# Kernel tuning notes

Measured on AMD Instinct MI355X. Metric: run time of the kernel, lower is better.

## Reference

```python
import jax, jax.numpy as jnp
import numpy as np

# dims
B, S, D, H, F = 4, 1024, 1024, 16, 4096
DH = D // H
THETA0 = 1.0   # base firing threshold of AdaptiveLIFNeuron
RHO = 0.9      # adaptation decay
EPS = 1e-5


def layer_norm(x, g, b):
    mu = jnp.mean(x, axis=-1, keepdims=True)
    var = jnp.mean((x - mu) ** 2, axis=-1, keepdims=True)
    return (x - mu) * jax.lax.rsqrt(var + EPS) * g + b


def spike(u):
    # Heaviside forward, sigmoid surrogate gradient (straight-through)
    sg = jax.nn.sigmoid(4.0 * u)
    hard = (u > 0).astype(u.dtype)
    return sg + jax.lax.stop_gradient(hard - sg)


def setup_inputs() -> dict:
    key = jax.random.key(0)
    ks = jax.random.split(key, 8)
    std = 0.02
    w = lambda k, shape: jax.random.normal(k, shape, jnp.float32) * std
    return {
        "x": jax.random.normal(ks[0], (B, S, D), jnp.float32),
        "Wq": w(ks[1], (D, D)), "bq": jnp.zeros((D,), jnp.float32),
        "Wk": w(ks[2], (D, D)), "bk": jnp.zeros((D,), jnp.float32),
        "Wv": w(ks[3], (D, D)), "bv": jnp.zeros((D,), jnp.float32),
        "Wo": w(ks[4], (D, D)), "bo": jnp.zeros((D,), jnp.float32),
        "g1": jnp.ones((D,), jnp.float32), "b1": jnp.zeros((D,), jnp.float32),
        "W1": w(ks[5], (D, F)), "bf1": jnp.zeros((F,), jnp.float32),
        "W2": w(ks[6], (F, D)), "bf2": jnp.zeros((D,), jnp.float32),
        "g2": jnp.ones((D,), jnp.float32), "b2": jnp.zeros((D,), jnp.float32),
        "decay": jnp.full((F,), 0.8, jnp.float32),  # per-feature membrane leak
        "beta": jnp.full((F,), 0.1, jnp.float32),   # per-feature threshold adaptation
    }


def reference(x, Wq, bq, Wk, bk, Wv, bv, Wo, bo, g1, b1, W1, bf1, W2, bf2, g2, b2, decay, beta):
    # --- causal multi-head self-attention (DSALayer) ---
    q = (x @ Wq + bq).reshape(B, S, H, DH)
    k = (x @ Wk + bk).reshape(B, S, H, DH)
    v = (x @ Wv + bv).reshape(B, S, H, DH)
    scores = jnp.einsum("bqhd,bkhd->bhqk", q, k) / np.sqrt(DH).astype(np.float32)
    causal = jnp.tril(jnp.ones((S, S), bool))
    scores = jnp.where(causal, scores, jnp.asarray(-1e9, scores.dtype))
    p = jax.nn.softmax(scores, axis=-1)
    attn = jnp.einsum("bhqk,bkhd->bqhd", p, v).reshape(B, S, D) @ Wo + bo
    h = layer_norm(x + attn, g1, b1)

    # --- feed-forward with per-timestep adaptive LIF recurrence ---
    ff = h @ W1 + bf1                      # [B, S, F]

    def step(carry, xt):
        vm, a = carry                      # membrane potential, adaptation
        vm = decay * vm + xt
        u = vm - (THETA0 + a)
        s = spike(u)
        vm = vm * (1.0 - s)                # hard reset on spike
        a = RHO * a + beta * s
        return (vm, a), s

    init = (jnp.zeros((B, F), x.dtype), jnp.zeros((B, F), x.dtype))
    _, spikes = jax.lax.scan(step, init, jnp.swapaxes(ff, 0, 1))  # scan over time
    spikes = jnp.swapaxes(spikes, 0, 1)    # [B, S, F]

    ff_out = spikes @ W2 + bf2
    return layer_norm(h + ff_out, g2, b2)
```

## Files before the change

### kernel.cpp

```cpp
#include <hip/hip_runtime.h>
#include <hip/hip_bf16.h>
#include <stdint.h>

#define Bsz 4
#define Ssz 1024
#define Dsz 1024
#define Hsz 16
#define Fsz 4096

typedef __hip_bfloat16 bf16;
typedef __attribute__((ext_vector_type(8))) short bf16x8;
typedef __attribute__((ext_vector_type(4))) float f32x4;

typedef __attribute__((address_space(1))) const void gvoid_t;
typedef __attribute__((address_space(3))) void svoid_t;

__device__ __forceinline__ void gload16(const bf16* g, bf16* l) {
    __builtin_amdgcn_global_load_lds((gvoid_t*)g, (svoid_t*)l, 16, 0, 0);
}

__global__ __launch_bounds__(256) void split_k(const float* __restrict__ src,
                                               bf16* __restrict__ hi,
                                               bf16* __restrict__ lo) {
    const int i = (blockIdx.x * 256 + threadIdx.x) * 4;
    const float4 v = *(const float4*)(src + i);
    float vv[4] = {v.x, v.y, v.z, v.w};
    #pragma unroll
    for (int u = 0; u < 4; ++u) {
        const bf16 h = __float2bfloat16(vv[u]);
        hi[i + u] = h;
        lo[i + u] = __float2bfloat16(vv[u] - __bfloat162float(h));
    }
}

__global__ __launch_bounds__(256) void transpose_split4_k(const float* __restrict__ Wq,
                                                          const float* __restrict__ Wk,
                                                          const float* __restrict__ Wv,
                                                          const float* __restrict__ Wo,
                                                          bf16* __restrict__ qkv_hi,
                                                          bf16* __restrict__ qkv_lo,
                                                          bf16* __restrict__ wo_hi,
                                                          bf16* __restrict__ wo_lo) {
    __shared__ float tile[32][33];
    const int z = blockIdx.z;
    const float* in = (z == 0) ? Wq : (z == 1) ? Wk : (z == 2) ? Wv : Wo;
    const size_t WP = (size_t)Dsz * Dsz;
    bf16* hiT = (z < 3) ? qkv_hi + (size_t)z * WP : wo_hi;
    bf16* loT = (z < 3) ? qkv_lo + (size_t)z * WP : wo_lo;
    const int bx = blockIdx.x * 32, by = blockIdx.y * 32;
    const int tx = threadIdx.x, ty = threadIdx.y;
    #pragma unroll
    for (int i = 0; i < 32; i += 8)
        tile[ty + i][tx] = in[(size_t)(by + ty + i) * Dsz + bx + tx];
    __syncthreads();
    #pragma unroll
    for (int i = 0; i < 32; i += 8) {
        const float v = tile[tx][ty + i];
        const bf16 h = __float2bfloat16(v);
        const size_t o = (size_t)(bx + ty + i) * Dsz + by + tx;
        hiT[o] = h;
        loT[o] = __float2bfloat16(v - __bfloat162float(h));
    }
}

__global__ __launch_bounds__(256) void transpose_split_k(const float* __restrict__ in,
                                                         bf16* __restrict__ hiT,
                                                         bf16* __restrict__ loT,
                                                         int R, int C) {
    __shared__ float tile[32][33];
    const int bx = blockIdx.x * 32, by = blockIdx.y * 32;
    const int tx = threadIdx.x, ty = threadIdx.y;
    #pragma unroll
    for (int i = 0; i < 32; i += 8)
        tile[ty + i][tx] = in[(size_t)(by + ty + i) * C + bx + tx];
    __syncthreads();
    #pragma unroll
    for (int i = 0; i < 32; i += 8) {
        const float v = tile[tx][ty + i];
        const bf16 h = __float2bfloat16(v);
        const size_t o = (size_t)(bx + ty + i) * R + by + tx;
        hiT[o] = h;
        loT[o] = __float2bfloat16(v - __bfloat162float(h));
    }
}

__global__ __launch_bounds__(256) void transpose_cast_k(const float* __restrict__ in,
                                                        bf16* __restrict__ outT,
                                                        int R, int C) {
    __shared__ float tile[32][33];
    const int bx = blockIdx.x * 32, by = blockIdx.y * 32;
    const int tx = threadIdx.x, ty = threadIdx.y;
    #pragma unroll
    for (int i = 0; i < 32; i += 8)
        tile[ty + i][tx] = in[(size_t)(by + ty + i) * C + bx + tx];
    __syncthreads();
    #pragma unroll
    for (int i = 0; i < 32; i += 8)
        outT[(size_t)(bx + ty + i) * R + by + tx] = __float2bfloat16(tile[tx][ty + i]);
}

__global__ __launch_bounds__(256) void gemm3_bt(const bf16* __restrict__ Ah,
                                                const bf16* __restrict__ Al,
                                                const bf16* __restrict__ Bh,
                                                const bf16* __restrict__ Bl,
                                                const float* __restrict__ bias,
                                                float* __restrict__ Cf,
                                                int M, int N, int K) {
    __shared__ alignas(16) bf16 Ash[128 * 32];
    __shared__ alignas(16) bf16 Asl[128 * 32];
    __shared__ alignas(16) bf16 Bsh[128 * 32];
    __shared__ alignas(16) bf16 Bsl[128 * 32];
    const int t = threadIdx.x;
    const int lane = t & 63, wv = t >> 6;
    const int mw = wv >> 1, nw = wv & 1;
    const int m0 = blockIdx.y * 128, n0 = blockIdx.x * 128;
    const int r16 = lane & 15, q8 = (lane >> 4) * 8;
    const int arow = t >> 2, acol = (t & 3) * 8;

    const bf16* gAh = Ah + (size_t)(m0 + arow) * K + acol;
    const bf16* gAl = Al + (size_t)(m0 + arow) * K + acol;
    const bf16* gBh = Bh + (size_t)(n0 + arow) * K + acol;
    const bf16* gBl = Bl + (size_t)(n0 + arow) * K + acol;
    const size_t rK64 = (size_t)64 * K;
    bf16* lAh = Ash + wv * 512;
    bf16* lAl = Asl + wv * 512;
    bf16* lBh = Bsh + wv * 512;
    bf16* lBl = Bsl + wv * 512;

    f32x4 acc[4][4] = {};

    for (int k0 = 0; k0 < K; k0 += 32) {
        __syncthreads();
        gload16(gAh + k0, lAh);  gload16(gAh + k0 + rK64, lAh + 2048);
        gload16(gAl + k0, lAl);  gload16(gAl + k0 + rK64, lAl + 2048);
        gload16(gBh + k0, lBh);  gload16(gBh + k0 + rK64, lBh + 2048);
        gload16(gBl + k0, lBl);  gload16(gBl + k0 + rK64, lBl + 2048);
        __syncthreads();

        bf16x8 ah[4], al[4], bh[4], bl[4];
        #pragma unroll
        for (int rt = 0; rt < 4; ++rt) {
            const int ro = (64 * mw + 16 * rt + r16) * 32 + q8;
            ah[rt] = *(const bf16x8*)(Ash + ro);
            al[rt] = *(const bf16x8*)(Asl + ro);
        }
        #pragma unroll
        for (int ct = 0; ct < 4; ++ct) {
            const int co = (64 * nw + 16 * ct + r16) * 32 + q8;
            bh[ct] = *(const bf16x8*)(Bsh + co);
            bl[ct] = *(const bf16x8*)(Bsl + co);
        }
        #pragma unroll
        for (int rt = 0; rt < 4; ++rt)
            #pragma unroll
            for (int ct = 0; ct < 4; ++ct) {
                acc[rt][ct] = __builtin_amdgcn_mfma_f32_16x16x32_bf16(ah[rt], bh[ct], acc[rt][ct], 0, 0, 0);
                acc[rt][ct] = __builtin_amdgcn_mfma_f32_16x16x32_bf16(ah[rt], bl[ct], acc[rt][ct], 0, 0, 0);
                acc[rt][ct] = __builtin_amdgcn_mfma_f32_16x16x32_bf16(al[rt], bh[ct], acc[rt][ct], 0, 0, 0);
            }
    }

    const int rowi = (lane >> 4) * 4;
    const int coli = lane & 15;
    #pragma unroll
    for (int ct = 0; ct < 4; ++ct) {
        const int col = n0 + 64 * nw + 16 * ct + coli;
        const float bv = bias[col];
        #pragma unroll
        for (int rt = 0; rt < 4; ++rt) {
            const int rowb = m0 + 64 * mw + 16 * rt + rowi;
            #pragma unroll
            for (int r = 0; r < 4; ++r)
                Cf[(size_t)(rowb + r) * N + col] = acc[rt][ct][r] + bv;
        }
    }
}

__global__ __launch_bounds__(256) void gemm3_qkv(const bf16* __restrict__ Ah,
                                                 const bf16* __restrict__ Al,
                                                 const bf16* __restrict__ Bh,
                                                 const bf16* __restrict__ Bl,
                                                 const float* __restrict__ bias,
                                                 bf16* __restrict__ qhi, bf16* __restrict__ qlo,
                                                 bf16* __restrict__ khi, bf16* __restrict__ klo,
                                                 bf16* __restrict__ vthi, bf16* __restrict__ vtlo) {
    const int K = Dsz;
    __shared__ alignas(16) bf16 Ash[128 * 32];
    __shared__ alignas(16) bf16 Asl[128 * 32];
    __shared__ alignas(16) bf16 Bsh[128 * 32];
    __shared__ alignas(16) bf16 Bsl[128 * 32];
    const int t = threadIdx.x;
    const int lane = t & 63, wv = t >> 6;
    const int mw = wv >> 1, nw = wv & 1;
    const int m0 = blockIdx.y * 128, n0 = blockIdx.x * 128;
    const int r16 = lane & 15, q8 = (lane >> 4) * 8;
    const int arow = t >> 2, acol = (t & 3) * 8;

    const bf16* gAh = Ah + (size_t)(m0 + arow) * K + acol;
    const bf16* gAl = Al + (size_t)(m0 + arow) * K + acol;
    const bf16* gBh = Bh + (size_t)(n0 + arow) * K + acol;
    const bf16* gBl = Bl + (size_t)(n0 + arow) * K + acol;
    const size_t rK64 = (size_t)64 * K;
    bf16* lAh = Ash + wv * 512;
    bf16* lAl = Asl + wv * 512;
    bf16* lBh = Bsh + wv * 512;
    bf16* lBl = Bsl + wv * 512;

    f32x4 acc[4][4] = {};

    for (int k0 = 0; k0 < K; k0 += 32) {
        __syncthreads();
        gload16(gAh + k0, lAh);  gload16(gAh + k0 + rK64, lAh + 2048);
        gload16(gAl + k0, lAl);  gload16(gAl + k0 + rK64, lAl + 2048);
        gload16(gBh + k0, lBh);  gload16(gBh + k0 + rK64, lBh + 2048);
        gload16(gBl + k0, lBl);  gload16(gBl + k0 + rK64, lBl + 2048);
        __syncthreads();

        bf16x8 ah[4], al[4], bh[4], bl[4];
        #pragma unroll
        for (int rt = 0; rt < 4; ++rt) {
            const int ro = (64 * mw + 16 * rt + r16) * 32 + q8;
            ah[rt] = *(const bf16x8*)(Ash + ro);
            al[rt] = *(const bf16x8*)(Asl + ro);
        }
        #pragma unroll
        for (int ct = 0; ct < 4; ++ct) {
            const int co = (64 * nw + 16 * ct + r16) * 32 + q8;
            bh[ct] = *(const bf16x8*)(Bsh + co);
            bl[ct] = *(const bf16x8*)(Bsl + co);
        }
        #pragma unroll
        for (int rt = 0; rt < 4; ++rt)
            #pragma unroll
            for (int ct = 0; ct < 4; ++ct) {
                acc[rt][ct] = __builtin_amdgcn_mfma_f32_16x16x32_bf16(ah[rt], bh[ct], acc[rt][ct], 0, 0, 0);
                acc[rt][ct] = __builtin_amdgcn_mfma_f32_16x16x32_bf16(ah[rt], bl[ct], acc[rt][ct], 0, 0, 0);
                acc[rt][ct] = __builtin_amdgcn_mfma_f32_16x16x32_bf16(al[rt], bh[ct], acc[rt][ct], 0, 0, 0);
            }
    }

    const int rowi = (lane >> 4) * 4;
    const int coli = lane & 15;
    if (n0 < 2048) {
        const float scale = (n0 < 1024) ? 0.125f : 1.0f;
        bf16* hip_ = (n0 < 1024) ? qhi : khi;
        bf16* lop_ = (n0 < 1024) ? qlo : klo;
        const int cbase = (n0 < 1024) ? n0 : (n0 - 1024);
        #pragma unroll
        for (int ct = 0; ct < 4; ++ct) {
            const int col = cbase + 64 * nw + 16 * ct + coli;
            const float bv = bias[n0 + 64 * nw + 16 * ct + coli];
            #pragma unroll
            for (int rt = 0; rt < 4; ++rt) {
                const int rowb = m0 + 64 * mw + 16 * rt + rowi;
                #pragma unroll
                for (int r = 0; r < 4; ++r) {
                    const float val = (acc[rt][ct][r] + bv) * scale;
                    const bf16 h = __float2bfloat16(val);
                    const size_t off = (size_t)(rowb + r) * Dsz + col;
                    hip_[off] = h;
                    lop_[off] = __float2bfloat16(val - __bfloat162float(h));
                }
            }
        }
    } else {
        #pragma unroll
        for (int ct = 0; ct < 4; ++ct) {
            const int col = n0 + 64 * nw + 16 * ct + coli;
            const float bv = bias[col];
            const int c2 = col - 2048;
            #pragma unroll
            for (int rt = 0; rt < 4; ++rt) {
                const int rowb = m0 + 64 * mw + 16 * rt + rowi;
                const int b = rowb >> 10, s = rowb & 1023;
                const size_t off = ((size_t)b * 16384 + (size_t)c2 * 1024) + s + 65536 * 0;
                bf16 hv[4], lv[4];
                #pragma unroll
                for (int r = 0; r < 4; ++r) {
                    const float val = acc[rt][ct][r] + bv;
                    hv[r] = __float2bfloat16(val);
                    lv[r] = __float2bfloat16(val - __bfloat162float(hv[r]));
                }
                const size_t vo = (size_t)b * (16 * 64 * 1024) + (size_t)c2 * 1024 + s;
                (void)off;
                *(uint2*)&vthi[vo] = *(const uint2*)hv;
                *(uint2*)&vtlo[vo] = *(const uint2*)lv;
            }
        }
    }
}

__global__ __launch_bounds__(256) void gemm1_bt(const bf16* __restrict__ A,
                                                const bf16* __restrict__ Bt,
                                                const float* __restrict__ bias,
                                                float* __restrict__ Cf,
                                                int M, int N, int K) {
    __shared__ alignas(16) bf16 As[128 * 32];
    __shared__ alignas(16) bf16 Bs[128 * 32];
    const int t = threadIdx.x;
    const int lane = t & 63, wv = t >> 6;
    const int mw = wv >> 1, nw = wv & 1;
    const int m0 = blockIdx.y * 128, n0 = blockIdx.x * 128;
    const int r16 = lane & 15, q8 = (lane >> 4) * 8;
    const int arow = t >> 2, acol = (t & 3) * 8;

    const bf16* gA = A + (size_t)(m0 + arow) * K + acol;
    const bf16* gB = Bt + (size_t)(n0 + arow) * K + acol;
    const size_t rK64 = (size_t)64 * K;
    bf16* lA = As + wv * 512;
    bf16* lB = Bs + wv * 512;

    f32x4 acc[4][4] = {};

    for (int k0 = 0; k0 < K; k0 += 32) {
        __syncthreads();
        gload16(gA + k0, lA);  gload16(gA + k0 + rK64, lA + 2048);
        gload16(gB + k0, lB);  gload16(gB + k0 + rK64, lB + 2048);
        __syncthreads();

        bf16x8 af[4], bf_[4];
        #pragma unroll
        for (int rt = 0; rt < 4; ++rt)
            af[rt] = *(const bf16x8*)(As + (64 * mw + 16 * rt + r16) * 32 + q8);
        #pragma unroll
        for (int ct = 0; ct < 4; ++ct)
            bf_[ct] = *(const bf16x8*)(Bs + (64 * nw + 16 * ct + r16) * 32 + q8);
        #pragma unroll
        for (int rt = 0; rt < 4; ++rt)
            #pragma unroll
            for (int ct = 0; ct < 4; ++ct)
                acc[rt][ct] = __builtin_amdgcn_mfma_f32_16x16x32_bf16(
                    af[rt], bf_[ct], acc[rt][ct], 0, 0, 0);
    }

    const int rowi = (lane >> 4) * 4;
    const int coli = lane & 15;
    #pragma unroll
    for (int ct = 0; ct < 4; ++ct) {
        const int col = n0 + 64 * nw + 16 * ct + coli;
        const float bv = bias[col];
        #pragma unroll
        for (int rt = 0; rt < 4; ++rt) {
            const int rowb = m0 + 64 * mw + 16 * rt + rowi;
            #pragma unroll
            for (int r = 0; r < 4; ++r)
                Cf[(size_t)(rowb + r) * N + col] = acc[rt][ct][r] + bv;
        }
    }
}

__global__ __launch_bounds__(256) void attn_mfma_k(const bf16* __restrict__ qhp,
                                                   const bf16* __restrict__ qlp,
                                                   const bf16* __restrict__ khp,
                                                   const bf16* __restrict__ klp,
                                                   const bf16* __restrict__ vhp,
                                                   const bf16* __restrict__ vlp,
                                                   bf16* __restrict__ ohi,
                                                   bf16* __restrict__ olo) {
    __shared__ alignas(16) bf16 Qh[64 * 72], Ql[64 * 72];
    __shared__ alignas(16) bf16 Kh[64 * 72], Kl[64 * 72];
    __shared__ alignas(16) bf16 Vh[64 * 72], Vl[64 * 72];
    __shared__ alignas(16) bf16 Ph[64 * 72], Pl[64 * 72];

    const int bh = blockIdx.y;
    const int b = bh >> 4, h = bh & 15;
    const int q0 = (gridDim.x - 1 - blockIdx.x) * 64;
    const int t = threadIdx.x, w = t >> 6, lane = t & 63;
    const int r16 = lane & 15, quad = lane >> 4;
    const int sr = t >> 2, sc = (t & 3) * 16;

    {
        const size_t g = (size_t)(b * Ssz + q0 + sr) * Dsz + h * 64 + sc;
        *(uint4*)&Qh[sr * 72 + sc]     = *(const uint4*)(qhp + g);
        *(uint4*)&Qh[sr * 72 + sc + 8] = *(const uint4*)(qhp + g + 8);
        *(uint4*)&Ql[sr * 72 + sc]     = *(const uint4*)(qlp + g);
        *(uint4*)&Ql[sr * 72 + sc + 8] = *(const uint4*)(qlp + g + 8);
    }

    f32x4 aco[4] = {};
    float lrun[4] = {0.f, 0.f, 0.f, 0.f};
    const int ntiles = q0 / 64 + 1;

    for (int kt = 0; kt < ntiles; ++kt) {
        __syncthreads();
        {
            const size_t g = (size_t)(b * Ssz + kt * 64 + sr) * Dsz + h * 64 + sc;
            *(uint4*)&Kh[sr * 72 + sc]     = *(const uint4*)(khp + g);
            *(uint4*)&Kh[sr * 72 + sc + 8] = *(const uint4*)(khp + g + 8);
            *(uint4*)&Kl[sr * 72 + sc]     = *(const uint4*)(klp + g);
            *(uint4*)&Kl[sr * 72 + sc + 8] = *(const uint4*)(klp + g + 8);
            const size_t gv = ((size_t)bh * 64 + sr) * Ssz + kt * 64 + sc;
            *(uint4*)&Vh[sr * 72 + sc]     = *(const uint4*)(vhp + gv);
            *(uint4*)&Vh[sr * 72 + sc + 8] = *(const uint4*)(vhp + gv + 8);
            *(uint4*)&Vl[sr * 72 + sc]     = *(const uint4*)(vlp + gv);
            *(uint4*)&Vl[sr * 72 + sc + 8] = *(const uint4*)(vlp + gv + 8);
        }
        __syncthreads();

        bf16x8 aQh[2], aQl[2];
        #pragma unroll
        for (int ks = 0; ks < 2; ++ks) {
            aQh[ks] = *(const bf16x8*)&Qh[(16 * w + r16) * 72 + ks * 32 + quad * 8];
            aQl[ks] = *(const bf16x8*)&Ql[(16 * w + r16) * 72 + ks * 32 + quad * 8];
        }
        #pragma unroll
        for (int nt = 0; nt < 4; ++nt) {
            f32x4 s = {};
            #pragma unroll
            for (int ks = 0; ks < 2; ++ks) {
                const bf16x8 bKh = *(const bf16x8*)&Kh[(16 * nt + r16) * 72 + ks * 32 + quad * 8];
                const bf16x8 bKl = *(const bf16x8*)&Kl[(16 * nt + r16) * 72 + ks * 32 + quad * 8];
                s = __builtin_amdgcn_mfma_f32_16x16x32_bf16(aQh[ks], bKh, s, 0, 0, 0);
                s = __builtin_amdgcn_mfma_f32_16x16x32_bf16(aQh[ks], bKl, s, 0, 0, 0);
                s = __builtin_amdgcn_mfma_f32_16x16x32_bf16(aQl[ks], bKh, s, 0, 0, 0);
            }
            const int key = kt * 64 + nt * 16 + r16;
            #pragma unroll
            for (int r = 0; r < 4; ++r) {
                const int qrow = q0 + 16 * w + quad * 4 + r;
                const float p = (key <= qrow) ? __expf(s[r]) : 0.f;
                lrun[r] += p;
                const bf16 ph = __float2bfloat16(p);
                Ph[(16 * w + quad * 4 + r) * 72 + nt * 16 + r16] = ph;
                Pl[(16 * w + quad * 4 + r) * 72 + nt * 16 + r16] =
                    __float2bfloat16(p - __bfloat162float(ph));
            }
        }

        bf16x8 aPh[2], aPl[2];
        #pragma unroll
        for (int ks = 0; ks < 2; ++ks) {
            aPh[ks] = *(const bf16x8*)&Ph[(16 * w + r16) * 72 + ks * 32 + quad * 8];
            aPl[ks] = *(const bf16x8*)&Pl[(16 * w + r16) * 72 + ks * 32 + quad * 8];
        }
        #pragma unroll
        for (int nt = 0; nt < 4; ++nt) {
            #pragma unroll
            for (int ks = 0; ks < 2; ++ks) {
                const bf16x8 bVh = *(const bf16x8*)&Vh[(16 * nt + r16) * 72 + ks * 32 + quad * 8];
                const bf16x8 bVl = *(const bf16x8*)&Vl[(16 * nt + r16) * 72 + ks * 32 + quad * 8];
                aco[nt] = __builtin_amdgcn_mfma_f32_16x16x32_bf16(aPh[ks], bVh, aco[nt], 0, 0, 0);
                aco[nt] = __builtin_amdgcn_mfma_f32_16x16x32_bf16(aPh[ks], bVl, aco[nt], 0, 0, 0);
                aco[nt] = __builtin_amdgcn_mfma_f32_16x16x32_bf16(aPl[ks], bVh, aco[nt], 0, 0, 0);
            }
        }
    }

    #pragma unroll
    for (int r = 0; r < 4; ++r) {
        float l = lrun[r];
        l += __shfl_xor(l, 1); l += __shfl_xor(l, 2);
        l += __shfl_xor(l, 4); l += __shfl_xor(l, 8);
        lrun[r] = l;
    }
    #pragma unroll
    for (int nt = 0; nt < 4; ++nt)
        #pragma unroll
        for (int r = 0; r < 4; ++r) {
            const size_t off = (size_t)(b * Ssz + q0 + 16 * w + quad * 4 + r) * Dsz
                               + h * 64 + nt * 16 + r16;
            const float val = aco[nt][r] / lrun[r];
            const bf16 hh = __float2bfloat16(val);
            ohi[off] = hh;
            olo[off] = __float2bfloat16(val - __bfloat162float(hh));
        }
}

__global__ __launch_bounds__(64) void scan_k(const float* __restrict__ ff,
                                             const float* __restrict__ decay,
                                             const float* __restrict__ beta,
                                             bf16* __restrict__ spikes) {
    const int idx = blockIdx.x * 64 + threadIdx.x;
    const int b = idx >> 12;
    const int f = idx & (Fsz - 1);
    const float dec = decay[f];
    const float bet = beta[f];
    const float* src = ff + (size_t)b * Ssz * Fsz + f;
    bf16* dst = spikes + (size_t)b * Ssz * Fsz + f;
    float vm = 0.f, a = 0.f;
    float buf[64];
    #pragma unroll
    for (int u = 0; u < 64; ++u) buf[u] = src[(size_t)u * Fsz];
    for (int gg = 0; gg < 16; ++gg) {
        #pragma unroll
        for (int sub = 0; sub < 4; ++sub) {
            const int g = gg * 4 + sub;
            #pragma unroll
            for (int u = 0; u < 16; ++u) {
                vm = dec * vm + buf[sub * 16 + u];
                const float uu = vm - (1.f + a);
                const float sp = (uu > 0.f) ? 1.f : 0.f;
                vm = (uu > 0.f) ? 0.f : vm;
                a = 0.9f * a + bet * sp;
                dst[(size_t)(g * 16 + u) * Fsz] = __float2bfloat16(sp);
            }
            if (g + 4 < 64) {
                #pragma unroll
                for (int u = 0; u < 16; ++u)
                    buf[sub * 16 + u] = src[(size_t)((g + 4) * 16 + u) * Fsz];
            }
        }
    }
}

__device__ __forceinline__ float block_sum(float val, float* ls, int t) {
    #pragma unroll
    for (int mm = 32; mm >= 1; mm >>= 1) val += __shfl_xor(val, mm);
    if ((t & 63) == 0) ls[t >> 6] = val;
    __syncthreads();
    const float r = ls[0] + ls[1] + ls[2] + ls[3];
    __syncthreads();
    return r;
}

__global__ __launch_bounds__(256) void ln1_k(const float* __restrict__ x,
                                             const float* __restrict__ ap,
                                             const float* __restrict__ g,
                                             const float* __restrict__ bb,
                                             bf16* __restrict__ h_hi,
                                             bf16* __restrict__ h_lo) {
    __shared__ float ls[4];
    const int row = blockIdx.x;
    const int t = threadIdx.x;
    const size_t base = (size_t)row * Dsz;
    float vv[4];
    #pragma unroll
    for (int i = 0; i < 4; ++i) {
        const int c = t + i * 256;
        vv[i] = x[base + c] + ap[base + c];
    }
    float s = vv[0] + vv[1] + vv[2] + vv[3];
    s = block_sum(s, ls, t);
    const float mu = s * (1.f / 1024.f);
    float qs = 0.f;
    #pragma unroll
    for (int i = 0; i < 4; ++i) { const float d = vv[i] - mu; qs += d * d; }
    qs = block_sum(qs, ls, t);
    const float rs = rsqrtf(qs * (1.f / 1024.f) + 1e-5f);
    #pragma unroll
    for (int i = 0; i < 4; ++i) {
        const int c = t + i * 256;
        const float o = (vv[i] - mu) * rs * g[c] + bb[c];
        const bf16 hi = __float2bfloat16(o);
        h_hi[base + c] = hi;
        h_lo[base + c] = __float2bfloat16(o - __bfloat162float(hi));
    }
}

__global__ __launch_bounds__(256) void ln2_k(const bf16* __restrict__ h_hi,
                                             const bf16* __restrict__ h_lo,
                                             const float* __restrict__ fo,
                                             const float* __restrict__ g,
                                             const float* __restrict__ bb,
                                             float* __restrict__ out) {
    __shared__ float ls[4];
    const int row = blockIdx.x;
    const int t = threadIdx.x;
    const size_t base = (size_t)row * Dsz;
    float vv[4];
    #pragma unroll
    for (int i = 0; i < 4; ++i) {
        const int c = t + i * 256;
        const float h = __bfloat162float(h_hi[base + c]) + __bfloat162float(h_lo[base + c]);
        vv[i] = h + fo[base + c];
    }
    float s = vv[0] + vv[1] + vv[2] + vv[3];
    s = block_sum(s, ls, t);
    const float mu = s * (1.f / 1024.f);
    float qs = 0.f;
    #pragma unroll
    for (int i = 0; i < 4; ++i) { const float d = vv[i] - mu; qs += d * d; }
    qs = block_sum(qs, ls, t);
    const float rs = rsqrtf(qs * (1.f / 1024.f) + 1e-5f);
    #pragma unroll
    for (int i = 0; i < 4; ++i) {
        const int c = t + i * 256;
        out[base + c] = (vv[i] - mu) * rs * g[c] + bb[c];
    }
}

extern "C" void kernel_launch(void* const* d_in, const int* in_sizes, int n_in,
                              void* d_out, int out_size, void* d_ws, size_t ws_size,
                              hipStream_t stream) {
    const float* x    = (const float*)d_in[0];
    const float* Wq   = (const float*)d_in[1];
    const float* bq   = (const float*)d_in[2];
    const float* Wk   = (const float*)d_in[3];
    const float* bk   = (const float*)d_in[4];
    const float* Wv   = (const float*)d_in[5];
    const float* bv   = (const float*)d_in[6];
    const float* Wo   = (const float*)d_in[7];
    const float* bo   = (const float*)d_in[8];
    const float* g1   = (const float*)d_in[9];
    const float* b1   = (const float*)d_in[10];
    const float* W1   = (const float*)d_in[11];
    const float* bf1  = (const float*)d_in[12];
    const float* W2   = (const float*)d_in[13];
    const float* bf2  = (const float*)d_in[14];
    const float* g2   = (const float*)d_in[15];
    const float* b2   = (const float*)d_in[16];
    const float* dec  = (const float*)d_in[17];
    const float* beta = (const float*)d_in[18];

    const size_t BSD = (size_t)Bsz * Ssz * Dsz;
    const size_t BSF = (size_t)Bsz * Ssz * Fsz;

    char* ws = (char*)d_ws;
    char* A3 = ws;
    char* A1 = A3 + BSF * 4;
    char* A2 = A1 + BSF * 2;
    char* A4 = A2 + (size_t)Dsz * Fsz * 2 * 2;
    float* bqkv = (float*)(A4 + BSD * 4);

    bf16* qhi   = (bf16*)(A3);
    bf16* qlo   = (bf16*)(A3 + BSD * 2);
    bf16* khi   = (bf16*)(A3 + BSD * 4);
    bf16* klo   = (bf16*)(A3 + BSD * 6);
    float* attnp = (float*)(A3 + BSD * 12);
    float* ffb   = (float*)(A3);
    float* ffout = (float*)(A3);

    bf16* xhi    = (bf16*)(A1);
    bf16* xlo    = (bf16*)(A1 + BSD * 2);
    bf16* athi   = (bf16*)(A1);
    bf16* atlo   = (bf16*)(A1 + BSD * 2);
    bf16* spikes = (bf16*)(A1);

    const size_t WP = (size_t)Dsz * Dsz;
    bf16* Wqkv_hi = (bf16*)(A2);
    bf16* Wqkv_lo = (bf16*)(A2 + WP * 3 * 2);
    bf16* WoThi   = (bf16*)(A2 + WP * 6 * 2);
    bf16* WoTlo   = (bf16*)(A2 + WP * 7 * 2);
    bf16* W1Thi   = (bf16*)(A2);
    bf16* W1Tlo   = (bf16*)(A2 + (size_t)Dsz * Fsz * 2);
    bf16* W2T     = (bf16*)(A2);

    bf16* vthi  = (bf16*)(A4);
    bf16* vtlo  = (bf16*)(A4 + BSD * 2);
    bf16* h_hi  = (bf16*)(A4);
    bf16* h_lo  = (bf16*)(A4 + BSD * 2);

    (void)ws_size; (void)in_sizes; (void)n_in; (void)out_size;

    const dim3 tb(32, 8);
    const int MBS = Bsz * Ssz;

    split_k<<<BSD / 1024, 256, 0, stream>>>(x, xhi, xlo);
    transpose_split4_k<<<dim3(32, 32, 4), tb, 0, stream>>>(
        Wq, Wk, Wv, Wo, Wqkv_hi, Wqkv_lo, WoThi, WoTlo);
    hipMemcpyAsync(bqkv,        (const void*)bq, Dsz * 4, hipMemcpyDeviceToDevice, stream);
    hipMemcpyAsync(bqkv + 1024, (const void*)bk, Dsz * 4, hipMemcpyDeviceToDevice, stream);
    hipMemcpyAsync(bqkv + 2048, (const void*)bv, Dsz * 4, hipMemcpyDeviceToDevice, stream);

    gemm3_qkv<<<dim3(3072 / 128, MBS / 128), 256, 0, stream>>>(
        xhi, xlo, Wqkv_hi, Wqkv_lo, bqkv, qhi, qlo, khi, klo, vthi, vtlo);

    attn_mfma_k<<<dim3(Ssz / 64, Bsz * Hsz), 256, 0, stream>>>(
        qhi, qlo, khi, klo, vthi, vtlo, athi, atlo);

    gemm3_bt<<<dim3(Dsz / 128, MBS / 128), 256, 0, stream>>>(
        athi, atlo, WoThi, WoTlo, bo, attnp, MBS, Dsz, Dsz);
    ln1_k<<<MBS, 256, 0, stream>>>(x, attnp, g1, b1, h_hi, h_lo);

    transpose_split_k<<<dim3(Fsz / 32, Dsz / 32), tb, 0, stream>>>(W1, W1Thi, W1Tlo, Dsz, Fsz);
    gemm3_bt<<<dim3(Fsz / 128, MBS / 128), 256, 0, stream>>>(
        h_hi, h_lo, W1Thi, W1Tlo, bf1, ffb, MBS, Fsz, Dsz);

    scan_k<<<Bsz * Fsz / 64, 64, 0, stream>>>(ffb, dec, beta, spikes);

    transpose_cast_k<<<dim3(Dsz / 32, Fsz / 32), tb, 0, stream>>>(W2, W2T, Fsz, Dsz);
    gemm1_bt<<<dim3(Dsz / 128, MBS / 128), 256, 0, stream>>>(
        spikes, W2T, bf2, ffout, MBS, Dsz, Fsz);

    ln2_k<<<MBS, 256, 0, stream>>>(h_hi, h_lo, ffout, g2, b2, (float*)d_out);
}
```

Baseline: 644.9 us.

## Split-K the Wo and W2 GEMMs, fold partial sums into LayerNorms, trim attention LDS

The Wo projection and the W2 GEMM (N=1024, 256 tiles) now launch with a split-K grid dimension of 2. Each half writes a separate fp32 partial buffer, with the bias added only by the first half, and the LayerNorm kernels sum the two partials as they read them. The goal is to fill more CUs on the MI355X, since 256 blocks underfill the device. Separately, the attention kernel keeps Q fragments in registers and stores P as fp32 in LDS, splitting it into hi/lo bf16 at read time, which cuts LDS footprint and may raise occupancy. The cost is an extra partial write and read per split GEMM, and the attention partial buffer now aliases the start of the workspace.

```diff
diff --git a/kernel.cpp b/kernel.cpp
--- a/kernel.cpp
+++ b/kernel.cpp
@@ -114,13 +114,15 @@
     const int lane = t & 63, wv = t >> 6;
     const int mw = wv >> 1, nw = wv & 1;
     const int m0 = blockIdx.y * 128, n0 = blockIdx.x * 128;
+    const int z = blockIdx.z, nz = gridDim.z;
+    const int Ks = K / nz, koff = z * Ks;
     const int r16 = lane & 15, q8 = (lane >> 4) * 8;
     const int arow = t >> 2, acol = (t & 3) * 8;
 
-    const bf16* gAh = Ah + (size_t)(m0 + arow) * K + acol;
-    const bf16* gAl = Al + (size_t)(m0 + arow) * K + acol;
-    const bf16* gBh = Bh + (size_t)(n0 + arow) * K + acol;
-    const bf16* gBl = Bl + (size_t)(n0 + arow) * K + acol;
+    const bf16* gAh = Ah + (size_t)(m0 + arow) * K + koff + acol;
+    const bf16* gAl = Al + (size_t)(m0 + arow) * K + koff + acol;
+    const bf16* gBh = Bh + (size_t)(n0 + arow) * K + koff + acol;
+    const bf16* gBl = Bl + (size_t)(n0 + arow) * K + koff + acol;
     const size_t rK64 = (size_t)64 * K;
     bf16* lAh = Ash + wv * 512;
     bf16* lAl = Asl + wv * 512;
@@ -129,7 +131,7 @@
 
     f32x4 acc[4][4] = {};
 
-    for (int k0 = 0; k0 < K; k0 += 32) {
+    for (int k0 = 0; k0 < Ks; k0 += 32) {
         __syncthreads();
         gload16(gAh + k0, lAh);  gload16(gAh + k0 + rK64, lAh + 2048);
         gload16(gAl + k0, lAl);  gload16(gAl + k0 + rK64, lAl + 2048);
@@ -160,18 +162,19 @@
             }
     }
 
+    float* Cz = Cf + (size_t)z * M * N;
     const int rowi = (lane >> 4) * 4;
     const int coli = lane & 15;
     #pragma unroll
     for (int ct = 0; ct < 4; ++ct) {
         const int col = n0 + 64 * nw + 16 * ct + coli;
-        const float bv = bias[col];
+        const float bv = (z == 0) ? bias[col] : 0.f;
         #pragma unroll
         for (int rt = 0; rt < 4; ++rt) {
             const int rowb = m0 + 64 * mw + 16 * rt + rowi;
             #pragma unroll
             for (int r = 0; r < 4; ++r)
-                Cf[(size_t)(rowb + r) * N + col] = acc[rt][ct][r] + bv;
+                Cz[(size_t)(rowb + r) * N + col] = acc[rt][ct][r] + bv;
         }
     }
 }
@@ -273,7 +276,6 @@
             for (int rt = 0; rt < 4; ++rt) {
                 const int rowb = m0 + 64 * mw + 16 * rt + rowi;
                 const int b = rowb >> 10, s = rowb & 1023;
-                const size_t off = ((size_t)b * 16384 + (size_t)c2 * 1024) + s + 65536 * 0;
                 bf16 hv[4], lv[4];
                 #pragma unroll
                 for (int r = 0; r < 4; ++r) {
@@ -282,7 +284,6 @@
                     lv[r] = __float2bfloat16(val - __bfloat162float(hv[r]));
                 }
                 const size_t vo = (size_t)b * (16 * 64 * 1024) + (size_t)c2 * 1024 + s;
-                (void)off;
                 *(uint2*)&vthi[vo] = *(const uint2*)hv;
                 *(uint2*)&vtlo[vo] = *(const uint2*)lv;
             }
@@ -301,18 +302,20 @@
     const int lane = t & 63, wv = t >> 6;
     const int mw = wv >> 1, nw = wv & 1;
     const int m0 = blockIdx.y * 128, n0 = blockIdx.x * 128;
+    const int z = blockIdx.z, nz = gridDim.z;
+    const int Ks = K / nz, koff = z * Ks;
     const int r16 = lane & 15, q8 = (lane >> 4) * 8;
     const int arow = t >> 2, acol = (t & 3) * 8;
 
-    const bf16* gA = A + (size_t)(m0 + arow) * K + acol;
-    const bf16* gB = Bt + (size_t)(n0 + arow) * K + acol;
+    const bf16* gA = A + (size_t)(m0 + arow) * K + koff + acol;
+    const bf16* gB = Bt + (size_t)(n0 + arow) * K + koff + acol;
     const size_t rK64 = (size_t)64 * K;
     bf16* lA = As + wv * 512;
     bf16* lB = Bs + wv * 512;
 
     f32x4 acc[4][4] = {};
 
-    for (int k0 = 0; k0 < K; k0 += 32) {
+    for (int k0 = 0; k0 < Ks; k0 += 32) {
         __syncthreads();
         gload16(gA + k0, lA);  gload16(gA + k0 + rK64, lA + 2048);
         gload16(gB + k0, lB);  gload16(gB + k0 + rK64, lB + 2048);
@@ -333,18 +336,19 @@
                     af[rt], bf_[ct], acc[rt][ct], 0, 0, 0);
     }
 
+    float* Cz = Cf + (size_t)z * M * N;
     const int rowi = (lane >> 4) * 4;
     const int coli = lane & 15;
     #pragma unroll
     for (int ct = 0; ct < 4; ++ct) {
         const int col = n0 + 64 * nw + 16 * ct + coli;
-        const float bv = bias[col];
+        const float bv = (z == 0) ? bias[col] : 0.f;
         #pragma unroll
         for (int rt = 0; rt < 4; ++rt) {
             const int rowb = m0 + 64 * mw + 16 * rt + rowi;
             #pragma unroll
             for (int r = 0; r < 4; ++r)
-                Cf[(size_t)(rowb + r) * N + col] = acc[rt][ct][r] + bv;
+                Cz[(size_t)(rowb + r) * N + col] = acc[rt][ct][r] + bv;
         }
     }
 }
@@ -357,10 +361,9 @@
                                                    const bf16* __restrict__ vlp,
                                                    bf16* __restrict__ ohi,
                                                    bf16* __restrict__ olo) {
-    __shared__ alignas(16) bf16 Qh[64 * 72], Ql[64 * 72];
+    __shared__ alignas(16) float Pf[64 * 68];
     __shared__ alignas(16) bf16 Kh[64 * 72], Kl[64 * 72];
     __shared__ alignas(16) bf16 Vh[64 * 72], Vl[64 * 72];
-    __shared__ alignas(16) bf16 Ph[64 * 72], Pl[64 * 72];
 
     const int bh = blockIdx.y;
     const int b = bh >> 4, h = bh & 15;
@@ -369,12 +372,13 @@
     const int r16 = lane & 15, quad = lane >> 4;
     const int sr = t >> 2, sc = (t & 3) * 16;
 
+    bf16x8 aQh[2], aQl[2];
     {
-        const size_t g = (size_t)(b * Ssz + q0 + sr) * Dsz + h * 64 + sc;
-        *(uint4*)&Qh[sr * 72 + sc]     = *(const uint4*)(qhp + g);
-        *(uint4*)&Qh[sr * 72 + sc + 8] = *(const uint4*)(qhp + g + 8);
-        *(uint4*)&Ql[sr * 72 + sc]     = *(const uint4*)(qlp + g);
-        *(uint4*)&Ql[sr * 72 + sc + 8] = *(const uint4*)(qlp + g + 8);
+        const size_t qb = (size_t)(b * Ssz + q0 + 16 * w + r16) * Dsz + h * 64 + quad * 8;
+        aQh[0] = *(const bf16x8*)(qhp + qb);
+        aQh[1] = *(const bf16x8*)(qhp + qb + 32);
+        aQl[0] = *(const bf16x8*)(qlp + qb);
+        aQl[1] = *(const bf16x8*)(qlp + qb + 32);
     }
 
     f32x4 aco[4] = {};
@@ -397,12 +401,6 @@
         }
         __syncthreads();
 
-        bf16x8 aQh[2], aQl[2];
-        #pragma unroll
-        for (int ks = 0; ks < 2; ++ks) {
-            aQh[ks] = *(const bf16x8*)&Qh[(16 * w + r16) * 72 + ks * 32 + quad * 8];
-            aQl[ks] = *(const bf16x8*)&Ql[(16 * w + r16) * 72 + ks * 32 + quad * 8];
-        }
         #pragma unroll
         for (int nt = 0; nt < 4; ++nt) {
             f32x4 s = {};
@@ -420,19 +418,26 @@
                 const int qrow = q0 + 16 * w + quad * 4 + r;
                 const float p = (key <= qrow) ? __expf(s[r]) : 0.f;
                 lrun[r] += p;
-                const bf16 ph = __float2bfloat16(p);
-                Ph[(16 * w + quad * 4 + r) * 72 + nt * 16 + r16] = ph;
-                Pl[(16 * w + quad * 4 + r) * 72 + nt * 16 + r16] =
-                    __float2bfloat16(p - __bfloat162float(ph));
+                Pf[(16 * w + quad * 4 + r) * 68 + nt * 16 + r16] = p;
             }
         }
 
         bf16x8 aPh[2], aPl[2];
         #pragma unroll
         for (int ks = 0; ks < 2; ++ks) {
-            aPh[ks] = *(const bf16x8*)&Ph[(16 * w + r16) * 72 + ks * 32 + quad * 8];
-            aPl[ks] = *(const bf16x8*)&Pl[(16 * w + r16) * 72 + ks * 32 + quad * 8];
-        }
+            const float4 pa = *(const float4*)&Pf[(16 * w + r16) * 68 + ks * 32 + quad * 8];
+            const float4 pb = *(const float4*)&Pf[(16 * w + r16) * 68 + ks * 32 + quad * 8 + 4];
+            const float pv[8] = {pa.x, pa.y, pa.z, pa.w, pb.x, pb.y, pb.z, pb.w};
+            bf16 hv[8], lv[8];
+            #pragma unroll
+            for (int j = 0; j < 8; ++j) {
+                hv[j] = __float2bfloat16(pv[j]);
+                lv[j] = __float2bfloat16(pv[j] - __bfloat162float(hv[j]));
+            }
+            aPh[ks] = *(const bf16x8*)hv;
+            aPl[ks] = *(const bf16x8*)lv;
+        }
+
         #pragma unroll
         for (int nt = 0; nt < 4; ++nt) {
             #pragma unroll
@@ -514,7 +519,8 @@
 }
 
 __global__ __launch_bounds__(256) void ln1_k(const float* __restrict__ x,
-                                             const float* __restrict__ ap,
+                                             const float* __restrict__ ap0,
+                                             const float* __restrict__ ap1,
                                              const float* __restrict__ g,
                                              const float* __restrict__ bb,
                                              bf16* __restrict__ h_hi,
@@ -527,7 +533,7 @@
     #pragma unroll
     for (int i = 0; i < 4; ++i) {
         const int c = t + i * 256;
-        vv[i] = x[base + c] + ap[base + c];
+        vv[i] = x[base + c] + (ap0[base + c] + ap1[base + c]);
     }
     float s = vv[0] + vv[1] + vv[2] + vv[3];
     s = block_sum(s, ls, t);
@@ -549,7 +555,8 @@
 
 __global__ __launch_bounds__(256) void ln2_k(const bf16* __restrict__ h_hi,
                                              const bf16* __restrict__ h_lo,
-                                             const float* __restrict__ fo,
+                                             const float* __restrict__ fo0,
+                                             const float* __restrict__ fo1,
                                              const float* __restrict__ g,
                                              const float* __restrict__ bb,
                                              float* __restrict__ out) {
@@ -562,7 +569,7 @@
     for (int i = 0; i < 4; ++i) {
         const int c = t + i * 256;
         const float h = __bfloat162float(h_hi[base + c]) + __bfloat162float(h_lo[base + c]);
-        vv[i] = h + fo[base + c];
+        vv[i] = h + (fo0[base + c] + fo1[base + c]);
     }
     float s = vv[0] + vv[1] + vv[2] + vv[3];
     s = block_sum(s, ls, t);
@@ -616,7 +623,7 @@
     bf16* qlo   = (bf16*)(A3 + BSD * 2);
     bf16* khi   = (bf16*)(A3 + BSD * 4);
     bf16* klo   = (bf16*)(A3 + BSD * 6);
-    float* attnp = (float*)(A3 + BSD * 12);
+    float* attnp = (float*)(A3);
     float* ffb   = (float*)(A3);
     float* ffout = (float*)(A3);
 
@@ -658,19 +665,21 @@
     attn_mfma_k<<<dim3(Ssz / 64, Bsz * Hsz), 256, 0, stream>>>(
         qhi, qlo, khi, klo, vthi, vtlo, athi, atlo);
 
-    gemm3_bt<<<dim3(Dsz / 128, MBS / 128), 256, 0, stream>>>(
+    gemm3_bt<<<dim3(Dsz / 128, MBS / 128, 2), 256, 0, stream>>>(
         athi, atlo, WoThi, WoTlo, bo, attnp, MBS, Dsz, Dsz);
-    ln1_k<<<MBS, 256, 0, stream>>>(x, attnp, g1, b1, h_hi, h_lo);
+    ln1_k<<<MBS, 256, 0, stream>>>(x, attnp, attnp + (size_t)MBS * Dsz,
+                                   g1, b1, h_hi, h_lo);
 
     transpose_split_k<<<dim3(Fsz / 32, Dsz / 32), tb, 0, stream>>>(W1, W1Thi, W1Tlo, Dsz, Fsz);
-    gemm3_bt<<<dim3(Fsz / 128, MBS / 128), 256, 0, stream>>>(
+    gemm3_bt<<<dim3(Fsz / 128, MBS / 128, 1), 256, 0, stream>>>(
         h_hi, h_lo, W1Thi, W1Tlo, bf1, ffb, MBS, Fsz, Dsz);
 
     scan_k<<<Bsz * Fsz / 64, 64, 0, stream>>>(ffb, dec, beta, spikes);
 
     transpose_cast_k<<<dim3(Dsz / 32, Fsz / 32), tb, 0, stream>>>(W2, W2T, Fsz, Dsz);
-    gemm1_bt<<<dim3(Dsz / 128, MBS / 128), 256, 0, stream>>>(
+    gemm1_bt<<<dim3(Dsz / 128, MBS / 128, 2), 256, 0, stream>>>(
         spikes, W2T, bf2, ffout, MBS, Dsz, Fsz);
 
-    ln2_k<<<MBS, 256, 0, stream>>>(h_hi, h_lo, ffout, g2, b2, (float*)d_out);
-}
+    ln2_k<<<MBS, 256, 0, stream>>>(h_hi, h_lo, ffout, ffout + (size_t)MBS * Dsz,
+                                   g2, b2, (float*)d_out);
+}
```

After: 624.0 us. -3.2%, faster.
